# Kernel tuning notes

Measured on AMD Instinct MI355X. Metric: run time of the kernel, lower is better.

Reference implementation:

```python
import jax, jax.numpy as jnp
import numpy as np

T, C, H, S = 2048, 2048, 32, 64
H_KV = 8
L_MAA, L_DEC = 32, 64


def setup_inputs() -> dict:
    key = jax.random.key(0)
    ks = jax.random.split(key, 20)
    def n(k, shp, s=1.0):
        return jax.random.normal(k, shp, dtype=jnp.float32) * s
    sc = 0.02  # init scale for projection weights
    return dict(
        x=n(ks[0], (T, C)),
        state=jnp.zeros((1 + S, C), jnp.float32),
        new_starts=jnp.zeros((T,), bool),
        length=T,
        time_maa_x=n(ks[1], (C,), 0.1),
        time_maa_r=n(ks[2], (C,), 0.1),
        time_maa_k=n(ks[3], (C,), 0.1),
        time_maa_v=n(ks[4], (C,), 0.1),
        time_maa_w=n(ks[5], (C,), 0.1),
        time_maa_g=n(ks[6], (C,), 0.1),
        time_maa_w1=n(ks[7], (C, 5 * L_MAA), sc),
        time_maa_w2=n(ks[8], (5, L_MAA, C), sc),
        time_decay=n(ks[9], (C,), 0.5),
        time_decay_w1=n(ks[10], (C, L_DEC), sc),
        time_decay_w2=n(ks[11], (L_DEC, C), sc),
        Wq=n(ks[12], (C, H * S), sc),
        Wk=n(ks[13], (C, H_KV * S), sc),
        Wv=n(ks[14], (C, H_KV * S), sc),
        Wg=n(ks[15], (C, C), sc),
        Wo=n(ks[16], (C, C), sc),
    )


def reference(x, state, new_starts, length,
              time_maa_x, time_maa_r, time_maa_k, time_maa_v, time_maa_w, time_maa_g,
              time_maa_w1, time_maa_w2,
              time_decay, time_decay_w1, time_decay_w2,
              Wq, Wk, Wv, Wg, Wo):
    # token shift: previous token (state[0] for t=0), zeroed at sequence starts
    sx = jnp.concatenate([state[:1], x[:-1]], axis=0)
    sx = jnp.where(new_starts[:, None], 0.0, sx) - x  # [T, C]

    # data-dependent token-shift mix via LoRA (5 branches: r,k,v,w,g)
    xxx = x + sx * time_maa_x
    m = jnp.tanh(xxx @ time_maa_w1).reshape(T, 5, L_MAA).transpose(1, 0, 2)  # [5,T,L]
    m = jnp.einsum('ntl,nlc->ntc', m, time_maa_w2)  # [5,T,C]
    mr, mk, mv, mw, mg = m
    xr = x + sx * (time_maa_r + mr)
    xk = x + sx * (time_maa_k + mk)
    xv = x + sx * (time_maa_v + mv)
    xw = x + sx * (time_maa_w + mw)
    xg = x + sx * (time_maa_g + mg)

    new_state0 = x[length - 1]  # last valid token

    r = (xr @ Wq).reshape(T, H, S)
    k = (xk @ Wk).reshape(T, H_KV, S)
    v = (xv @ Wv).reshape(T, H_KV, S)

    # per-token decay via LoRA
    dec = time_decay.reshape(1, H, S) + (jnp.tanh(xw @ time_decay_w1) @ time_decay_w2).reshape(T, H, S)
    g = jax.nn.sigmoid(xg @ Wg)  # [T, C]

    reps = H // H_KV
    k = jnp.repeat(k, reps, axis=1)  # [T,H,S]
    v = jnp.repeat(v, reps, axis=1)

    log_w = jnp.maximum(-jnp.exp(dec), -5.0)  # [T,H,S]
    k = k * (1.0 - jnp.exp(log_w))

    s0 = state[1:].reshape(H, S, S)

    def step(s, inp):
        r_t, k_t, v_t, lw_t, ns_t = inp
        s = jnp.where(ns_t, 0.0, s)
        # decay along key dim, then rank-1 update k^T v
        s = s * jnp.exp(lw_t)[:, :, None] + k_t[:, :, None] * v_t[:, None, :]
        o = jnp.einsum('hk,hkv->hv', r_t, s)
        return s, o

    s_fin, out = jax.lax.scan(step, s0, (r, k, v, log_w, new_starts))

    new_state = state.at[0].set(new_state0).at[1:].set(s_fin.reshape(S, H * S))
    y = out.reshape(T, H * S) * g
    return y @ Wo, new_state
```

## Files before the change

### kernel.cpp

```cpp
#include <hip/hip_runtime.h>
#include <hip/hip_bf16.h>
#include <cmath>

#define T_DIM 2048
#define C_DIM 2048
#define NH    32
#define SS    64
#define NC    64
#define CL    32

typedef unsigned short ushort_t;
typedef __attribute__((ext_vector_type(8))) short bf16x8;
typedef __attribute__((ext_vector_type(4))) float f32x4;

__device__ __forceinline__ ushort_t f2bf(float v) {
    union { __hip_bfloat16 b; ushort_t u; } cv;
    cv.b = __float2bfloat16(v);
    return cv.u;
}

__device__ __forceinline__ void gload_lds16(const void* g, void* l) {
    __builtin_amdgcn_global_load_lds((const __attribute__((address_space(1))) void*)g,
                                     (__attribute__((address_space(3))) void*)l,
                                     16, 0, 0);
}

__device__ __forceinline__ float bcast(float x, int k) {
    return __int_as_float(__builtin_amdgcn_readlane(__float_as_int(x), k));
}

__global__ __launch_bounds__(256)
void mega_init(const float* __restrict__ W1, const float* __restrict__ Wd1,
               const float* __restrict__ Wd2, const float* __restrict__ Wq,
               const float* __restrict__ Wk, const float* __restrict__ Wv,
               const float* __restrict__ Wg, const float* __restrict__ W2,
               ushort_t* __restrict__ W1T, ushort_t* __restrict__ Wd1T,
               ushort_t* __restrict__ Wd2T, ushort_t* __restrict__ WqT,
               ushort_t* __restrict__ WkT, ushort_t* __restrict__ WvT,
               ushort_t* __restrict__ WgT, ushort_t* __restrict__ W2Tall,
               const float* __restrict__ x, const float* __restrict__ state,
               const unsigned char* __restrict__ ns, const float* __restrict__ tmx,
               float* __restrict__ sx, ushort_t* __restrict__ xxxb,
               const int* __restrict__ len, float* __restrict__ outstate) {
    __shared__ float t[32][33];
    int bx = blockIdx.x;
    int tid = threadIdx.x;

    if (bx < 4096) {
        int i4 = bx * 256 + tid;
        int idx = i4 * 4;
        int tt = idx >> 11;
        int c = idx & 2047;
        float4 xv = *(const float4*)(x + idx);
        float4 prev;
        if (ns[tt]) prev = make_float4(0.f, 0.f, 0.f, 0.f);
        else if (tt == 0) prev = *(const float4*)(state + c);
        else prev = *(const float4*)(x + idx - C_DIM);
        float4 tm = *(const float4*)(tmx + c);
        float4 s4;
        s4.x = prev.x - xv.x;  s4.y = prev.y - xv.y;
        s4.z = prev.z - xv.z;  s4.w = prev.w - xv.w;
        *(float4*)(sx + idx) = s4;
        ushort4 xb;
        xb.x = f2bf(xv.x + s4.x * tm.x);
        xb.y = f2bf(xv.y + s4.y * tm.y);
        xb.z = f2bf(xv.z + s4.z * tm.z);
        xb.w = f2bf(xv.w + s4.w * tm.w);
        *(ushort4*)(xxxb + idx) = xb;
        return;
    }
    bx -= 4096;
    if (bx < 8) {
        int c = bx * 256 + tid;
        if (c < C_DIM)
            outstate[c] = x[(size_t)(len[0] - 1) * C_DIM + c];
        return;
    }
    bx -= 8;
    const float* W; ushort_t* WT; int K, N, nx;
    if (bx < 512)        {            W = W1;  WT = W1T;  K = 2048; N = 160;  nx = 8;  }
    else if (bx < 768)   { bx -= 512; W = Wd1; WT = Wd1T; K = 2048; N = 64;   nx = 4;  }
    else if (bx < 896)   { bx -= 768; W = Wd2; WT = Wd2T; K = 64;   N = 2048; nx = 64; }
    else if (bx < 4992)  { bx -= 896; W = Wq;  WT = WqT;  K = 2048; N = 2048; nx = 64; }
    else if (bx < 6016)  { bx -= 4992; W = Wk; WT = WkT;  K = 2048; N = 512;  nx = 16; }
    else if (bx < 7040)  { bx -= 6016; W = Wv; WT = WvT;  K = 2048; N = 512;  nx = 16; }
    else if (bx < 11136) { bx -= 7040; W = Wg; WT = WgT;  K = 2048; N = 2048; nx = 64; }
    else {
        bx -= 11136;
        int br = bx >> 6; bx &= 63;
        W = W2 + (size_t)br * 32 * C_DIM; WT = W2Tall + (size_t)br * C_DIM * 32;
        K = 32; N = 2048; nx = 64;
    }
    int n0 = (bx % nx) * 32, k0 = (bx / nx) * 32;
    int tx = tid & 31, ty = tid >> 5;
    #pragma unroll
    for (int i = 0; i < 4; ++i) {
        int k = ty + i * 8;
        float v = 0.f;
        if (n0 + tx < N) v = W[(size_t)(k0 + k) * N + n0 + tx];
        t[k][tx] = v;
    }
    __syncthreads();
    #pragma unroll
    for (int i = 0; i < 4; ++i) {
        int n = ty + i * 8;
        WT[(size_t)(n0 + n) * K + k0 + tx] = f2bf(t[tx][n]);
    }
}

template<int EPI>
__global__ __launch_bounds__(256)
void gemm_mfma(const ushort_t* __restrict__ A, int lda,
               const ushort_t* __restrict__ BT,
               const float* __restrict__ bias,
               float* __restrict__ Cf, ushort_t* __restrict__ Cb,
               int ldc, int K) {
    __shared__ ushort_t As[2][128 * 32];
    __shared__ ushort_t Bs[2][128 * 32];
    int tid = threadIdx.x;
    int wave = tid >> 6, lane = tid & 63;
    int m0 = blockIdx.y * 128, n0 = blockIdx.x * 128;
    int wm = wave >> 1, wn = wave & 1;

    f32x4 acc[4][4] = {};

    int srow0 = wave * 16 + (lane >> 2);
    int schunk = lane & 3;

    int row0 = srow0, row1 = 64 + srow0;
    int gch0 = schunk ^ (row0 & 3), gch1 = schunk ^ (row1 & 3);
    const ushort_t* gA0 = A + (size_t)(m0 + row0) * lda + gch0 * 8;
    const ushort_t* gA1 = A + (size_t)(m0 + row1) * lda + gch1 * 8;
    const ushort_t* gB0 = BT + (size_t)(n0 + row0) * K + gch0 * 8;
    const ushort_t* gB1 = BT + (size_t)(n0 + row1) * K + gch1 * 8;
    int l0 = row0 * 32 + schunk * 8;
    int l1 = row1 * 32 + schunk * 8;

    int nt = K >> 5;

    gload_lds16(gA0, &As[0][l0]);
    gload_lds16(gB0, &Bs[0][l0]);
    gload_lds16(gA1, &As[0][l1]);
    gload_lds16(gB1, &Bs[0][l1]);
    __syncthreads();

    int fr = lane & 15;
    int fc = lane >> 4;
    int cur = 0;
    for (int t = 0; t < nt; ++t) {
        if (t + 1 < nt) {
            int k0 = (t + 1) << 5;
            gload_lds16(gA0 + k0, &As[cur ^ 1][l0]);
            gload_lds16(gB0 + k0, &Bs[cur ^ 1][l0]);
            gload_lds16(gA1 + k0, &As[cur ^ 1][l1]);
            gload_lds16(gB1 + k0, &Bs[cur ^ 1][l1]);
        }
        bf16x8 af[4], bfr[4];
        #pragma unroll
        for (int mi = 0; mi < 4; ++mi) {
            int r = wm * 64 + mi * 16 + fr;
            af[mi] = *(const bf16x8*)(&As[cur][r * 32 + ((fc ^ (r & 3)) * 8)]);
        }
        #pragma unroll
        for (int ni = 0; ni < 4; ++ni) {
            int c = wn * 64 + ni * 16 + fr;
            bfr[ni] = *(const bf16x8*)(&Bs[cur][c * 32 + ((fc ^ (c & 3)) * 8)]);
        }
        #pragma unroll
        for (int mi = 0; mi < 4; ++mi)
            #pragma unroll
            for (int ni = 0; ni < 4; ++ni)
                acc[mi][ni] = __builtin_amdgcn_mfma_f32_16x16x32_bf16(
                    af[mi], bfr[ni], acc[mi][ni], 0, 0, 0);
        __syncthreads();
        cur ^= 1;
    }

    int colin = lane & 15;
    int rquad = lane >> 4;
    #pragma unroll
    for (int mi = 0; mi < 4; ++mi) {
        #pragma unroll
        for (int reg = 0; reg < 4; ++reg) {
            int row = m0 + wm * 64 + mi * 16 + rquad * 4 + reg;
            #pragma unroll
            for (int ni = 0; ni < 4; ++ni) {
                int col = n0 + wn * 64 + ni * 16 + colin;
                float v = acc[mi][ni][reg];
                if (EPI == 2) v = 1.f / (1.f + __expf(-v));
                else if (EPI == 3) v += bias[col];
                else if (EPI == 4) v = tanhf(v);
                if (EPI == 4) Cb[(size_t)row * ldc + col] = f2bf(v);
                else          Cf[(size_t)row * ldc + col] = v;
            }
        }
    }
}

__global__ __launch_bounds__(256)
void gemm_fused5(const ushort_t* __restrict__ xw, const ushort_t* __restrict__ xk,
                 const ushort_t* __restrict__ xv, const ushort_t* __restrict__ xr,
                 const ushort_t* __restrict__ xg,
                 const ushort_t* __restrict__ Wd1T, const ushort_t* __restrict__ WkT,
                 const ushort_t* __restrict__ WvT, const ushort_t* __restrict__ WqT,
                 const ushort_t* __restrict__ WgT,
                 ushort_t* __restrict__ tw, float* __restrict__ k0g,
                 float* __restrict__ v0g, float* __restrict__ rg,
                 float* __restrict__ gg) {
    const int K = 2048, lda = 2048;
    int id = blockIdx.y * 41 + blockIdx.x;
    int swz = (id & 7) * 82 + (id >> 3);
    int bx = swz >> 4;
    int m0 = (swz & 15) * 128;

    const ushort_t* A; const ushort_t* BT;
    float* Cf = nullptr; ushort_t* Cb = nullptr;
    int ldc, n0, epi;
    if (bx == 0)       { A = xw; BT = Wd1T; Cb = tw;  ldc = 128;  n0 = 0;               epi = 4; }
    else if (bx < 5)   { A = xk; BT = WkT;  Cf = k0g; ldc = 512;  n0 = (bx - 1) * 128;  epi = 0; }
    else if (bx < 9)   { A = xv; BT = WvT;  Cf = v0g; ldc = 512;  n0 = (bx - 5) * 128;  epi = 0; }
    else if (bx < 25)  { A = xr; BT = WqT;  Cf = rg;  ldc = 2048; n0 = (bx - 9) * 128;  epi = 0; }
    else               { A = xg; BT = WgT;  Cf = gg;  ldc = 2048; n0 = (bx - 25) * 128; epi = 2; }

    __shared__ ushort_t As[2][128 * 32];
    __shared__ ushort_t Bs[2][128 * 32];
    int tid = threadIdx.x;
    int wave = tid >> 6, lane = tid & 63;
    int wm = wave >> 1, wn = wave & 1;

    f32x4 acc[4][4] = {};

    int srow0 = wave * 16 + (lane >> 2);
    int schunk = lane & 3;
    int row0 = srow0, row1 = 64 + srow0;
    int gch0 = schunk ^ (row0 & 3), gch1 = schunk ^ (row1 & 3);
    const ushort_t* gA0 = A + (size_t)(m0 + row0) * lda + gch0 * 8;
    const ushort_t* gA1 = A + (size_t)(m0 + row1) * lda + gch1 * 8;
    const ushort_t* gB0 = BT + (size_t)(n0 + row0) * K + gch0 * 8;
    const ushort_t* gB1 = BT + (size_t)(n0 + row1) * K + gch1 * 8;
    int l0 = row0 * 32 + schunk * 8;
    int l1 = row1 * 32 + schunk * 8;

    const int nt = K >> 5;
    gload_lds16(gA0, &As[0][l0]);
    gload_lds16(gB0, &Bs[0][l0]);
    gload_lds16(gA1, &As[0][l1]);
    gload_lds16(gB1, &Bs[0][l1]);
    __syncthreads();

    int fr = lane & 15;
    int fc = lane >> 4;
    int cur = 0;
    for (int t = 0; t < nt; ++t) {
        if (t + 1 < nt) {
            int kk = (t + 1) << 5;
            gload_lds16(gA0 + kk, &As[cur ^ 1][l0]);
            gload_lds16(gB0 + kk, &Bs[cur ^ 1][l0]);
            gload_lds16(gA1 + kk, &As[cur ^ 1][l1]);
            gload_lds16(gB1 + kk, &Bs[cur ^ 1][l1]);
        }
        bf16x8 af[4], bfr[4];
        #pragma unroll
        for (int mi = 0; mi < 4; ++mi) {
            int r = wm * 64 + mi * 16 + fr;
            af[mi] = *(const bf16x8*)(&As[cur][r * 32 + ((fc ^ (r & 3)) * 8)]);
        }
        #pragma unroll
        for (int ni = 0; ni < 4; ++ni) {
            int c = wn * 64 + ni * 16 + fr;
            bfr[ni] = *(const bf16x8*)(&Bs[cur][c * 32 + ((fc ^ (c & 3)) * 8)]);
        }
        #pragma unroll
        for (int mi = 0; mi < 4; ++mi)
            #pragma unroll
            for (int ni = 0; ni < 4; ++ni)
                acc[mi][ni] = __builtin_amdgcn_mfma_f32_16x16x32_bf16(
                    af[mi], bfr[ni], acc[mi][ni], 0, 0, 0);
        __syncthreads();
        cur ^= 1;
    }

    int colin = lane & 15;
    int rquad = lane >> 4;
    #pragma unroll
    for (int mi = 0; mi < 4; ++mi) {
        #pragma unroll
        for (int reg = 0; reg < 4; ++reg) {
            int row = m0 + wm * 64 + mi * 16 + rquad * 4 + reg;
            #pragma unroll
            for (int ni = 0; ni < 4; ++ni) {
                int col = n0 + wn * 64 + ni * 16 + colin;
                float v = acc[mi][ni][reg];
                if (epi == 2) v = 1.f / (1.f + __expf(-v));
                else if (epi == 4) v = tanhf(v);
                if (epi == 4) Cb[(size_t)row * ldc + col] = f2bf(v);
                else          Cf[(size_t)row * ldc + col] = v;
            }
        }
    }
}

__global__ __launch_bounds__(256)
void dec_cast(const ushort_t* __restrict__ tw, const ushort_t* __restrict__ Wd2T,
              const float* __restrict__ tdec, float* __restrict__ dec,
              const float* __restrict__ Wo, ushort_t* __restrict__ WoT) {
    int id = blockIdx.x;
    int tid = threadIdx.x;
    if (id >= 256) {
        __shared__ float t[32][33];
        int c = id - 256;
        int n0 = (c & 63) * 32, k0 = (c >> 6) * 32;
        int tx = tid & 31, ty = tid >> 5;
        #pragma unroll
        for (int i = 0; i < 4; ++i) {
            int k = ty + i * 8;
            t[k][tx] = Wo[(size_t)(k0 + k) * 2048 + n0 + tx];
        }
        __syncthreads();
        #pragma unroll
        for (int i = 0; i < 4; ++i) {
            int n = ty + i * 8;
            WoT[(size_t)(n0 + n) * 2048 + k0 + tx] = f2bf(t[tx][n]);
        }
        return;
    }
    const int K = 64, lda = 128, ldc = 2048;
    __shared__ ushort_t As[2][128 * 32];
    __shared__ ushort_t Bs[2][128 * 32];
    int wave = tid >> 6, lane = tid & 63;
    int m0 = (id >> 4) * 128, n0 = (id & 15) * 128;
    int wm = wave >> 1, wn = wave & 1;

    f32x4 acc[4][4] = {};
    int srow0 = wave * 16 + (lane >> 2);
    int schunk = lane & 3;
    int row0 = srow0, row1 = 64 + srow0;
    int gch0 = schunk ^ (row0 & 3), gch1 = schunk ^ (row1 & 3);
    const ushort_t* gA0 = tw + (size_t)(m0 + row0) * lda + gch0 * 8;
    const ushort_t* gA1 = tw + (size_t)(m0 + row1) * lda + gch1 * 8;
    const ushort_t* gB0 = Wd2T + (size_t)(n0 + row0) * K + gch0 * 8;
    const ushort_t* gB1 = Wd2T + (size_t)(n0 + row1) * K + gch1 * 8;
    int l0 = row0 * 32 + schunk * 8;
    int l1 = row1 * 32 + schunk * 8;

    const int nt = K >> 5;
    gload_lds16(gA0, &As[0][l0]);
    gload_lds16(gB0, &Bs[0][l0]);
    gload_lds16(gA1, &As[0][l1]);
    gload_lds16(gB1, &Bs[0][l1]);
    __syncthreads();

    int fr = lane & 15;
    int fc = lane >> 4;
    int cur = 0;
    for (int t = 0; t < nt; ++t) {
        if (t + 1 < nt) {
            int kk = (t + 1) << 5;
            gload_lds16(gA0 + kk, &As[cur ^ 1][l0]);
            gload_lds16(gB0 + kk, &Bs[cur ^ 1][l0]);
            gload_lds16(gA1 + kk, &As[cur ^ 1][l1]);
            gload_lds16(gB1 + kk, &Bs[cur ^ 1][l1]);
        }
        bf16x8 af[4], bfr[4];
        #pragma unroll
        for (int mi = 0; mi < 4; ++mi) {
            int r = wm * 64 + mi * 16 + fr;
            af[mi] = *(const bf16x8*)(&As[cur][r * 32 + ((fc ^ (r & 3)) * 8)]);
        }
        #pragma unroll
        for (int ni = 0; ni < 4; ++ni) {
            int c = wn * 64 + ni * 16 + fr;
            bfr[ni] = *(const bf16x8*)(&Bs[cur][c * 32 + ((fc ^ (c & 3)) * 8)]);
        }
        #pragma unroll
        for (int mi = 0; mi < 4; ++mi)
            #pragma unroll
            for (int ni = 0; ni < 4; ++ni)
                acc[mi][ni] = __builtin_amdgcn_mfma_f32_16x16x32_bf16(
                    af[mi], bfr[ni], acc[mi][ni], 0, 0, 0);
        __syncthreads();
        cur ^= 1;
    }

    int colin = lane & 15;
    int rquad = lane >> 4;
    #pragma unroll
    for (int mi = 0; mi < 4; ++mi) {
        #pragma unroll
        for (int reg = 0; reg < 4; ++reg) {
            int row = m0 + wm * 64 + mi * 16 + rquad * 4 + reg;
            #pragma unroll
            for (int ni = 0; ni < 4; ++ni) {
                int col = n0 + wn * 64 + ni * 16 + colin;
                dec[(size_t)row * ldc + col] = acc[mi][ni][reg] + tdec[col];
            }
        }
    }
}

__global__ __launch_bounds__(256)
void maa_gemm(const ushort_t* __restrict__ mtlb,
              const ushort_t* __restrict__ W2Tall,
              const float* __restrict__ x, const float* __restrict__ sx,
              const float* __restrict__ tmr, const float* __restrict__ tmk,
              const float* __restrict__ tmv, const float* __restrict__ tmw,
              const float* __restrict__ tmg,
              ushort_t* __restrict__ xr, ushort_t* __restrict__ xk,
              ushort_t* __restrict__ xv, ushort_t* __restrict__ xw,
              ushort_t* __restrict__ xg) {
    int br = blockIdx.z;
    const ushort_t* BT = W2Tall + (size_t)br * C_DIM * 32;
    const float* tm; ushort_t* dst;
    if      (br == 0) { tm = tmr; dst = xr; }
    else if (br == 1) { tm = tmk; dst = xk; }
    else if (br == 2) { tm = tmv; dst = xv; }
    else if (br == 3) { tm = tmw; dst = xw; }
    else              { tm = tmg; dst = xg; }

    __shared__ ushort_t As[128 * 32];
    __shared__ ushort_t Bs[128 * 32];
    int tid = threadIdx.x;
    int wave = tid >> 6, lane = tid & 63;
    int m0 = blockIdx.y * 128, n0 = blockIdx.x * 128;
    int wm = wave >> 1, wn = wave & 1;
    int srow0 = wave * 16 + (lane >> 2);
    int schunk = lane & 3;

    #pragma unroll
    for (int j = 0; j < 2; ++j) {
        int row = j * 64 + srow0;
        int gch = schunk ^ (row & 3);
        gload_lds16(mtlb + (size_t)(m0 + row) * 256 + br * 32 + gch * 8,
                    As + row * 32 + schunk * 8);
        gload_lds16(BT + (size_t)(n0 + row) * 32 + gch * 8,
                    Bs + row * 32 + schunk * 8);
    }
    __syncthreads();

    int fr = lane & 15;
    int fc = lane >> 4;
    f32x4 acc[4][4] = {};
    bf16x8 af[4], bfr[4];
    #pragma unroll
    for (int mi = 0; mi < 4; ++mi) {
        int r = wm * 64 + mi * 16 + fr;
        af[mi] = *(const bf16x8*)(As + r * 32 + ((fc ^ (r & 3)) * 8));
    }
    #pragma unroll
    for (int ni = 0; ni < 4; ++ni) {
        int c = wn * 64 + ni * 16 + fr;
        bfr[ni] = *(const bf16x8*)(Bs + c * 32 + ((fc ^ (c & 3)) * 8));
    }
    #pragma unroll
    for (int mi = 0; mi < 4; ++mi)
        #pragma unroll
        for (int ni = 0; ni < 4; ++ni)
            acc[mi][ni] = __builtin_amdgcn_mfma_f32_16x16x32_bf16(
                af[mi], bfr[ni], acc[mi][ni], 0, 0, 0);

    int colin = lane & 15;
    int rquad = lane >> 4;
    #pragma unroll
    for (int mi = 0; mi < 4; ++mi) {
        #pragma unroll
        for (int reg = 0; reg < 4; ++reg) {
            int row = m0 + wm * 64 + mi * 16 + rquad * 4 + reg;
            #pragma unroll
            for (int ni = 0; ni < 4; ++ni) {
                int col = n0 + wn * 64 + ni * 16 + colin;
                size_t idx = (size_t)row * C_DIM + col;
                float m = acc[mi][ni][reg];
                dst[idx] = f2bf(x[idx] + sx[idx] * (tm[col] + m));
            }
        }
    }
}

__global__ __launch_bounds__(64)
void scan_pass1(const float* __restrict__ k0, const float* __restrict__ v0,
                const float* __restrict__ dec, const unsigned char* __restrict__ ns,
                float* __restrict__ U, float* __restrict__ P) {
    int h = blockIdx.x, c = blockIdx.y, v = threadIdx.x;
    int hk = h >> 2;
    float u[64];
    #pragma unroll
    for (int k = 0; k < 64; ++k) u[k] = 0.f;
    float pk = 1.f;
    int t0 = c * CL;
    float dv_n = dec[(size_t)t0 * 2048 + h * 64 + v];
    float kv_n = k0[(size_t)t0 * 512 + hk * 64 + v];
    float vv_n = v0[(size_t)t0 * 512 + hk * 64 + v];
    unsigned char ns_n = ns[t0];
    for (int i = 0; i < CL; ++i) {
        float dv = dv_n, kv = kv_n, vv = vv_n;
        unsigned char nsv = ns_n;
        if (i + 1 < CL) {
            int t = t0 + i + 1;
            dv_n = dec[(size_t)t * 2048 + h * 64 + v];
            kv_n = k0[(size_t)t * 512 + hk * 64 + v];
            vv_n = v0[(size_t)t * 512 + hk * 64 + v];
            ns_n = ns[t];
        }
        float lw = fmaxf(-__expf(dv), -5.f);
        float ew = __expf(lw);
        float ewp = nsv ? 0.f : ew;
        float kk = kv * (1.f - ew);
        pk *= ewp;
        #pragma unroll
        for (int k = 0; k < 64; ++k) {
            float ewk = bcast(ewp, k);
            float kkk = bcast(kk, k);
            u[k] = fmaf(u[k], ewk, kkk * vv);
        }
    }
    size_t base = ((size_t)h * NC + c) * 4096;
    #pragma unroll
    for (int k = 0; k < 64; ++k) U[base + k * 64 + v] = u[k];
    P[((size_t)h * NC + c) * 64 + v] = pk;
}

__global__ __launch_bounds__(256)
void scan_pass2(float* __restrict__ U, const float* __restrict__ P,
                const float* __restrict__ state, float* __restrict__ outstate) {
    int e = blockIdx.x * 256 + threadIdx.x;
    int h = e >> 12;
    int k = (e >> 6) & 63;
    float s = state[C_DIM + e];
    int rem = e & 4095;
    #pragma unroll 4
    for (int c = 0; c < NC; ++c) {
        size_t ub = ((size_t)h * NC + c) * 4096 + rem;
        float p = P[((size_t)h * NC + c) * 64 + k];
        float u = U[ub];
        U[ub] = s;
        s = fmaf(s, p, u);
    }
    outstate[C_DIM + e] = s;
}

__global__ __launch_bounds__(64)
void scan_pass3(const float* __restrict__ r, const float* __restrict__ k0,
                const float* __restrict__ v0, const float* __restrict__ dec,
                const unsigned char* __restrict__ ns,
                const float* __restrict__ Sstarts, const float* __restrict__ g,
                ushort_t* __restrict__ y0b) {
    int h = blockIdx.x, c = blockIdx.y, v = threadIdx.x;
    int hk = h >> 2;
    float s[64];
    size_t base = ((size_t)h * NC + c) * 4096;
    #pragma unroll
    for (int k = 0; k < 64; ++k) s[k] = Sstarts[base + k * 64 + v];
    int t0 = c * CL;
    float dv_n = dec[(size_t)t0 * 2048 + h * 64 + v];
    float kv_n = k0[(size_t)t0 * 512 + hk * 64 + v];
    float vv_n = v0[(size_t)t0 * 512 + hk * 64 + v];
    float rr_n = r[(size_t)t0 * 2048 + h * 64 + v];
    float gg_n = g[(size_t)t0 * 2048 + h * 64 + v];
    unsigned char ns_n = ns[t0];
    for (int i = 0; i < CL; ++i) {
        float dv = dv_n, kv = kv_n, vv = vv_n, rr = rr_n, gg = gg_n;
        unsigned char nsv = ns_n;
        if (i + 1 < CL) {
            int t = t0 + i + 1;
            dv_n = dec[(size_t)t * 2048 + h * 64 + v];
            kv_n = k0[(size_t)t * 512 + hk * 64 + v];
            vv_n = v0[(size_t)t * 512 + hk * 64 + v];
            rr_n = r[(size_t)t * 2048 + h * 64 + v];
            gg_n = g[(size_t)t * 2048 + h * 64 + v];
            ns_n = ns[t];
        }
        float lw = fmaxf(-__expf(dv), -5.f);
        float ew = __expf(lw);
        float ewl = nsv ? 0.f : ew;
        float kkl = kv * (1.f - ew);
        float o0 = 0.f, o1 = 0.f, o2 = 0.f, o3 = 0.f;
        #pragma unroll
        for (int k = 0; k < 64; k += 4) {
            float s0 = fmaf(s[k],     bcast(ewl, k),     bcast(kkl, k)     * vv); s[k]     = s0; o0 = fmaf(bcast(rr, k),     s0, o0);
            float s1 = fmaf(s[k + 1], bcast(ewl, k + 1), bcast(kkl, k + 1) * vv); s[k + 1] = s1; o1 = fmaf(bcast(rr, k + 1), s1, o1);
            float s2 = fmaf(s[k + 2], bcast(ewl, k + 2), bcast(kkl, k + 2) * vv); s[k + 2] = s2; o2 = fmaf(bcast(rr, k + 2), s2, o2);
            float s3 = fmaf(s[k + 3], bcast(ewl, k + 3), bcast(kkl, k + 3) * vv); s[k + 3] = s3; o3 = fmaf(bcast(rr, k + 3), s3, o3);
        }
        float o = (o0 + o1) + (o2 + o3);
        size_t idx = (size_t)(t0 + i) * 2048 + h * 64 + v;
        y0b[idx] = f2bf(o * gg);
    }
}

extern "C" void kernel_launch(void* const* d_in, const int* in_sizes, int n_in,
                              void* d_out, int out_size, void* d_ws, size_t ws_size,
                              hipStream_t stream) {
    const float* x     = (const float*)d_in[0];
    const float* state = (const float*)d_in[1];
    const unsigned char* ns = (const unsigned char*)d_in[2];
    const int*   len   = (const int*)d_in[3];
    const float* tmx   = (const float*)d_in[4];
    const float* tmr   = (const float*)d_in[5];
    const float* tmk   = (const float*)d_in[6];
    const float* tmv   = (const float*)d_in[7];
    const float* tmw   = (const float*)d_in[8];
    const float* tmg   = (const float*)d_in[9];
    const float* W1    = (const float*)d_in[10];
    const float* W2    = (const float*)d_in[11];
    const float* tdec  = (const float*)d_in[12];
    const float* Wd1   = (const float*)d_in[13];
    const float* Wd2   = (const float*)d_in[14];
    const float* Wq    = (const float*)d_in[15];
    const float* Wk    = (const float*)d_in[16];
    const float* Wv    = (const float*)d_in[17];
    const float* Wg    = (const float*)d_in[18];
    const float* Wo    = (const float*)d_in[19];

    float* out = (float*)d_out;
    float* outstate = out + (size_t)T_DIM * C_DIM;

    char* wsb = (char*)d_ws;
    const size_t MB = 1024 * 1024;
    float*    sx   = (float*)(wsb + 0);
    float*    g    = (float*)(wsb + 0);
    ushort_t* xxxb = (ushort_t*)(wsb + 16 * MB);
    ushort_t* mtlb = (ushort_t*)(wsb + 24 * MB);
    ushort_t* tw   = (ushort_t*)(wsb + 25 * MB);
    float*    P    = (float*)(wsb + 25 * MB + 512 * 1024);
    ushort_t* xr   = (ushort_t*)(wsb + 26 * MB);
    ushort_t* xk   = (ushort_t*)(wsb + 34 * MB);
    float*    dec  = (float*)(wsb + 26 * MB);
    ushort_t* xv   = (ushort_t*)(wsb + 42 * MB);
    ushort_t* WoT  = (ushort_t*)(wsb + 42 * MB);
    ushort_t* xw   = (ushort_t*)(wsb + 50 * MB);
    ushort_t* xg   = (ushort_t*)(wsb + 58 * MB);
    float*    r    = (float*)(wsb + 66 * MB);
    float*    k0   = (float*)(wsb + 82 * MB);
    float*    v0   = (float*)(wsb + 86 * MB);
    ushort_t* WqT  = (ushort_t*)(wsb + 90 * MB);
    ushort_t* WkT  = (ushort_t*)(wsb + 98 * MB);
    ushort_t* WvT  = (ushort_t*)(wsb + 100 * MB);
    ushort_t* W1T  = (ushort_t*)(wsb + 102 * MB);
    ushort_t* Wd1T = (ushort_t*)(wsb + 103 * MB);
    ushort_t* Wd2T = (ushort_t*)(wsb + 103 * MB + 512 * 1024);
    ushort_t* W2Tall = (ushort_t*)(wsb + 104 * MB);
    ushort_t* WgT  = (ushort_t*)(wsb + 106 * MB);
    float*    U    = (float*)(wsb + 90 * MB);
    ushort_t* y0b  = xxxb;

    dim3 blk(256);

    mega_init<<<dim3(15560), blk, 0, stream>>>(
        W1, Wd1, Wd2, Wq, Wk, Wv, Wg, W2,
        W1T, Wd1T, Wd2T, WqT, WkT, WvT, WgT, W2Tall,
        x, state, ns, tmx, sx, xxxb, len, outstate);

    gemm_mfma<4><<<dim3(2, 16), blk, 0, stream>>>(xxxb, 2048, W1T, nullptr, nullptr, mtlb, 256, 2048);
    maa_gemm<<<dim3(16, 16, 5), blk, 0, stream>>>(mtlb, W2Tall, x, sx,
                                                  tmr, tmk, tmv, tmw, tmg,
                                                  xr, xk, xv, xw, xg);
    gemm_fused5<<<dim3(41, 16), blk, 0, stream>>>(xw, xk, xv, xr, xg,
                                                  Wd1T, WkT, WvT, WqT, WgT,
                                                  tw, k0, v0, r, g);
    dec_cast<<<dim3(4352), blk, 0, stream>>>(tw, Wd2T, tdec, dec, Wo, WoT);
    scan_pass1<<<dim3(NH, NC), dim3(64), 0, stream>>>(k0, v0, dec, ns, U, P);
    scan_pass2<<<dim3(512), blk, 0, stream>>>(U, P, state, outstate);
    scan_pass3<<<dim3(NH, NC), dim3(64), 0, stream>>>(r, k0, v0, dec, ns, U, g, y0b);
    gemm_mfma<0><<<dim3(16, 16), blk, 0, stream>>>(y0b, 2048, WoT, nullptr, out, nullptr, 2048, 2048);
}
```

Baseline: 474.1 us.

## Split-K the W1 LoRA GEMM, retile Wo GEMM blocks by XCD, change LDS swizzle

The small W1 GEMM (2048x256, K=2048) previously ran on only 32 blocks. It is now split along K into 8 slices writing fp32 partials, followed by a reduce kernel that sums the slices and applies tanh with a bf16 cast. This is meant to fill the GPU with more blocks. The Wo GEMM gets a block-index remap that groups tiles per XCD for L2 locality, and every GEMM switches to a new XOR swizzle for LDS reads to cut bank conflicts. The cost is extra partial traffic plus one more kernel launch.

```diff
diff --git a/kernel.cpp b/kernel.cpp
--- a/kernel.cpp
+++ b/kernel.cpp
@@ -8,6 +8,8 @@
 #define SS    64
 #define NC    64
 #define CL    32
+
+#define SWZ(r) (((r) + ((r) >> 2)) & 3)
 
 typedef unsigned short ushort_t;
 typedef __attribute__((ext_vector_type(8))) short bf16x8;
@@ -108,27 +110,120 @@
     }
 }
 
-template<int EPI>
 __global__ __launch_bounds__(256)
-void gemm_mfma(const ushort_t* __restrict__ A, int lda,
+void w1_splitk(const ushort_t* __restrict__ A,
                const ushort_t* __restrict__ BT,
-               const float* __restrict__ bias,
-               float* __restrict__ Cf, ushort_t* __restrict__ Cb,
-               int ldc, int K) {
+               float* __restrict__ Wp) {
+    const int lda = 2048, K = 2048;
     __shared__ ushort_t As[2][128 * 32];
     __shared__ ushort_t Bs[2][128 * 32];
     int tid = threadIdx.x;
     int wave = tid >> 6, lane = tid & 63;
     int m0 = blockIdx.y * 128, n0 = blockIdx.x * 128;
+    int kbase = blockIdx.z * 256;
+    float* Cf = Wp + (size_t)blockIdx.z * 2048 * 256;
     int wm = wave >> 1, wn = wave & 1;
 
     f32x4 acc[4][4] = {};
-
     int srow0 = wave * 16 + (lane >> 2);
     int schunk = lane & 3;
-
     int row0 = srow0, row1 = 64 + srow0;
-    int gch0 = schunk ^ (row0 & 3), gch1 = schunk ^ (row1 & 3);
+    int gch0 = schunk ^ SWZ(row0), gch1 = schunk ^ SWZ(row1);
+    const ushort_t* gA0 = A + (size_t)(m0 + row0) * lda + kbase + gch0 * 8;
+    const ushort_t* gA1 = A + (size_t)(m0 + row1) * lda + kbase + gch1 * 8;
+    const ushort_t* gB0 = BT + (size_t)(n0 + row0) * K + kbase + gch0 * 8;
+    const ushort_t* gB1 = BT + (size_t)(n0 + row1) * K + kbase + gch1 * 8;
+    int l0 = row0 * 32 + schunk * 8;
+    int l1 = row1 * 32 + schunk * 8;
+
+    const int nt = 8;
+    gload_lds16(gA0, &As[0][l0]);
+    gload_lds16(gB0, &Bs[0][l0]);
+    gload_lds16(gA1, &As[0][l1]);
+    gload_lds16(gB1, &Bs[0][l1]);
+    __syncthreads();
+
+    int fr = lane & 15;
+    int fc = lane >> 4;
+    int cur = 0;
+    for (int t = 0; t < nt; ++t) {
+        if (t + 1 < nt) {
+            int kk = (t + 1) << 5;
+            gload_lds16(gA0 + kk, &As[cur ^ 1][l0]);
+            gload_lds16(gB0 + kk, &Bs[cur ^ 1][l0]);
+            gload_lds16(gA1 + kk, &As[cur ^ 1][l1]);
+            gload_lds16(gB1 + kk, &Bs[cur ^ 1][l1]);
+        }
+        bf16x8 af[4], bfr[4];
+        #pragma unroll
+        for (int mi = 0; mi < 4; ++mi) {
+            int r = wm * 64 + mi * 16 + fr;
+            af[mi] = *(const bf16x8*)(&As[cur][r * 32 + ((fc ^ SWZ(r)) * 8)]);
+        }
+        #pragma unroll
+        for (int ni = 0; ni < 4; ++ni) {
+            int c = wn * 64 + ni * 16 + fr;
+            bfr[ni] = *(const bf16x8*)(&Bs[cur][c * 32 + ((fc ^ SWZ(c)) * 8)]);
+        }
+        #pragma unroll
+        for (int mi = 0; mi < 4; ++mi)
+            #pragma unroll
+            for (int ni = 0; ni < 4; ++ni)
+                acc[mi][ni] = __builtin_amdgcn_mfma_f32_16x16x32_bf16(
+                    af[mi], bfr[ni], acc[mi][ni], 0, 0, 0);
+        __syncthreads();
+        cur ^= 1;
+    }
+
+    int colin = lane & 15;
+    int rquad = lane >> 4;
+    #pragma unroll
+    for (int mi = 0; mi < 4; ++mi)
+        #pragma unroll
+        for (int reg = 0; reg < 4; ++reg) {
+            int row = m0 + wm * 64 + mi * 16 + rquad * 4 + reg;
+            #pragma unroll
+            for (int ni = 0; ni < 4; ++ni) {
+                int col = n0 + wn * 64 + ni * 16 + colin;
+                Cf[(size_t)row * 256 + col] = acc[mi][ni][reg];
+            }
+        }
+}
+
+__global__ __launch_bounds__(256)
+void w1_reduce(const float* __restrict__ Wp, ushort_t* __restrict__ mtlb) {
+    int idx = (blockIdx.x * 256 + threadIdx.x) * 4;
+    float4 s = *(const float4*)(Wp + idx);
+    #pragma unroll
+    for (int z = 1; z < 8; ++z) {
+        float4 p = *(const float4*)(Wp + (size_t)z * 2048 * 256 + idx);
+        s.x += p.x; s.y += p.y; s.z += p.z; s.w += p.w;
+    }
+    ushort4 o;
+    o.x = f2bf(tanhf(s.x)); o.y = f2bf(tanhf(s.y));
+    o.z = f2bf(tanhf(s.z)); o.w = f2bf(tanhf(s.w));
+    *(ushort4*)(mtlb + idx) = o;
+}
+
+__global__ __launch_bounds__(256)
+void gemm_wo(const ushort_t* __restrict__ A, const ushort_t* __restrict__ BT,
+             float* __restrict__ Cf) {
+    const int lda = 2048, K = 2048, ldc = 2048;
+    __shared__ ushort_t As[2][128 * 32];
+    __shared__ ushort_t Bs[2][128 * 32];
+    int tid = threadIdx.x;
+    int wave = tid >> 6, lane = tid & 63;
+    int id = blockIdx.y * 16 + blockIdx.x;
+    int xcd = id & 7, j = id >> 3;
+    int m0 = ((xcd >> 1) * 4 + (j & 3)) * 128;
+    int n0 = ((xcd & 1) * 8 + (j >> 2)) * 128;
+    int wm = wave >> 1, wn = wave & 1;
+
+    f32x4 acc[4][4] = {};
+    int srow0 = wave * 16 + (lane >> 2);
+    int schunk = lane & 3;
+    int row0 = srow0, row1 = 64 + srow0;
+    int gch0 = schunk ^ SWZ(row0), gch1 = schunk ^ SWZ(row1);
     const ushort_t* gA0 = A + (size_t)(m0 + row0) * lda + gch0 * 8;
     const ushort_t* gA1 = A + (size_t)(m0 + row1) * lda + gch1 * 8;
     const ushort_t* gB0 = BT + (size_t)(n0 + row0) * K + gch0 * 8;
@@ -136,8 +231,7 @@
     int l0 = row0 * 32 + schunk * 8;
     int l1 = row1 * 32 + schunk * 8;
 
-    int nt = K >> 5;
-
+    const int nt = K >> 5;
     gload_lds16(gA0, &As[0][l0]);
     gload_lds16(gB0, &Bs[0][l0]);
     gload_lds16(gA1, &As[0][l1]);
@@ -149,22 +243,22 @@
     int cur = 0;
     for (int t = 0; t < nt; ++t) {
         if (t + 1 < nt) {
-            int k0 = (t + 1) << 5;
-            gload_lds16(gA0 + k0, &As[cur ^ 1][l0]);
-            gload_lds16(gB0 + k0, &Bs[cur ^ 1][l0]);
-            gload_lds16(gA1 + k0, &As[cur ^ 1][l1]);
-            gload_lds16(gB1 + k0, &Bs[cur ^ 1][l1]);
+            int kk = (t + 1) << 5;
+            gload_lds16(gA0 + kk, &As[cur ^ 1][l0]);
+            gload_lds16(gB0 + kk, &Bs[cur ^ 1][l0]);
+            gload_lds16(gA1 + kk, &As[cur ^ 1][l1]);
+            gload_lds16(gB1 + kk, &Bs[cur ^ 1][l1]);
         }
         bf16x8 af[4], bfr[4];
         #pragma unroll
         for (int mi = 0; mi < 4; ++mi) {
             int r = wm * 64 + mi * 16 + fr;
-            af[mi] = *(const bf16x8*)(&As[cur][r * 32 + ((fc ^ (r & 3)) * 8)]);
+            af[mi] = *(const bf16x8*)(&As[cur][r * 32 + ((fc ^ SWZ(r)) * 8)]);
         }
         #pragma unroll
         for (int ni = 0; ni < 4; ++ni) {
             int c = wn * 64 + ni * 16 + fr;
-            bfr[ni] = *(const bf16x8*)(&Bs[cur][c * 32 + ((fc ^ (c & 3)) * 8)]);
+            bfr[ni] = *(const bf16x8*)(&Bs[cur][c * 32 + ((fc ^ SWZ(c)) * 8)]);
         }
         #pragma unroll
         for (int mi = 0; mi < 4; ++mi)
@@ -179,22 +273,16 @@
     int colin = lane & 15;
     int rquad = lane >> 4;
     #pragma unroll
-    for (int mi = 0; mi < 4; ++mi) {
+    for (int mi = 0; mi < 4; ++mi)
         #pragma unroll
         for (int reg = 0; reg < 4; ++reg) {
             int row = m0 + wm * 64 + mi * 16 + rquad * 4 + reg;
             #pragma unroll
             for (int ni = 0; ni < 4; ++ni) {
                 int col = n0 + wn * 64 + ni * 16 + colin;
-                float v = acc[mi][ni][reg];
-                if (EPI == 2) v = 1.f / (1.f + __expf(-v));
-                else if (EPI == 3) v += bias[col];
-                else if (EPI == 4) v = tanhf(v);
-                if (EPI == 4) Cb[(size_t)row * ldc + col] = f2bf(v);
-                else          Cf[(size_t)row * ldc + col] = v;
+                Cf[(size_t)row * ldc + col] = acc[mi][ni][reg];
             }
         }
-    }
 }
 
 __global__ __launch_bounds__(256)
@@ -229,11 +317,10 @@
     int wm = wave >> 1, wn = wave & 1;
 
     f32x4 acc[4][4] = {};
-
     int srow0 = wave * 16 + (lane >> 2);
     int schunk = lane & 3;
     int row0 = srow0, row1 = 64 + srow0;
-    int gch0 = schunk ^ (row0 & 3), gch1 = schunk ^ (row1 & 3);
+    int gch0 = schunk ^ SWZ(row0), gch1 = schunk ^ SWZ(row1);
     const ushort_t* gA0 = A + (size_t)(m0 + row0) * lda + gch0 * 8;
     const ushort_t* gA1 = A + (size_t)(m0 + row1) * lda + gch1 * 8;
     const ushort_t* gB0 = BT + (size_t)(n0 + row0) * K + gch0 * 8;
@@ -263,12 +350,12 @@
         #pragma unroll
         for (int mi = 0; mi < 4; ++mi) {
             int r = wm * 64 + mi * 16 + fr;
-            af[mi] = *(const bf16x8*)(&As[cur][r * 32 + ((fc ^ (r & 3)) * 8)]);
+            af[mi] = *(const bf16x8*)(&As[cur][r * 32 + ((fc ^ SWZ(r)) * 8)]);
         }
         #pragma unroll
         for (int ni = 0; ni < 4; ++ni) {
             int c = wn * 64 + ni * 16 + fr;
-            bfr[ni] = *(const bf16x8*)(&Bs[cur][c * 32 + ((fc ^ (c & 3)) * 8)]);
+            bfr[ni] = *(const bf16x8*)(&Bs[cur][c * 32 + ((fc ^ SWZ(c)) * 8)]);
         }
         #pragma unroll
         for (int mi = 0; mi < 4; ++mi)
@@ -335,7 +422,7 @@
     int srow0 = wave * 16 + (lane >> 2);
     int schunk = lane & 3;
     int row0 = srow0, row1 = 64 + srow0;
-    int gch0 = schunk ^ (row0 & 3), gch1 = schunk ^ (row1 & 3);
+    int gch0 = schunk ^ SWZ(row0), gch1 = schunk ^ SWZ(row1);
     const ushort_t* gA0 = tw + (size_t)(m0 + row0) * lda + gch0 * 8;
     const ushort_t* gA1 = tw + (size_t)(m0 + row1) * lda + gch1 * 8;
     const ushort_t* gB0 = Wd2T + (size_t)(n0 + row0) * K + gch0 * 8;
@@ -365,12 +452,12 @@
         #pragma unroll
         for (int mi = 0; mi < 4; ++mi) {
             int r = wm * 64 + mi * 16 + fr;
-            af[mi] = *(const bf16x8*)(&As[cur][r * 32 + ((fc ^ (r & 3)) * 8)]);
+            af[mi] = *(const bf16x8*)(&As[cur][r * 32 + ((fc ^ SWZ(r)) * 8)]);
         }
         #pragma unroll
         for (int ni = 0; ni < 4; ++ni) {
             int c = wn * 64 + ni * 16 + fr;
-            bfr[ni] = *(const bf16x8*)(&Bs[cur][c * 32 + ((fc ^ (c & 3)) * 8)]);
+            bfr[ni] = *(const bf16x8*)(&Bs[cur][c * 32 + ((fc ^ SWZ(c)) * 8)]);
         }
         #pragma unroll
         for (int mi = 0; mi < 4; ++mi)
@@ -385,7 +472,7 @@
     int colin = lane & 15;
     int rquad = lane >> 4;
     #pragma unroll
-    for (int mi = 0; mi < 4; ++mi) {
+    for (int mi = 0; mi < 4; ++mi)
         #pragma unroll
         for (int reg = 0; reg < 4; ++reg) {
             int row = m0 + wm * 64 + mi * 16 + rquad * 4 + reg;
@@ -395,7 +482,6 @@
                 dec[(size_t)row * ldc + col] = acc[mi][ni][reg] + tdec[col];
             }
         }
-    }
 }
 
 __global__ __launch_bounds__(256)
@@ -429,7 +515,7 @@
     #pragma unroll
     for (int j = 0; j < 2; ++j) {
         int row = j * 64 + srow0;
-        int gch = schunk ^ (row & 3);
+        int gch = schunk ^ SWZ(row);
         gload_lds16(mtlb + (size_t)(m0 + row) * 256 + br * 32 + gch * 8,
                     As + row * 32 + schunk * 8);
         gload_lds16(BT + (size_t)(n0 + row) * 32 + gch * 8,
@@ -444,12 +530,12 @@
     #pragma unroll
     for (int mi = 0; mi < 4; ++mi) {
         int r = wm * 64 + mi * 16 + fr;
-        af[mi] = *(const bf16x8*)(As + r * 32 + ((fc ^ (r & 3)) * 8));
+        af[mi] = *(const bf16x8*)(As + r * 32 + ((fc ^ SWZ(r)) * 8));
     }
     #pragma unroll
     for (int ni = 0; ni < 4; ++ni) {
         int c = wn * 64 + ni * 16 + fr;
-        bfr[ni] = *(const bf16x8*)(Bs + c * 32 + ((fc ^ (c & 3)) * 8));
+        bfr[ni] = *(const bf16x8*)(Bs + c * 32 + ((fc ^ SWZ(c)) * 8));
     }
     #pragma unroll
     for (int mi = 0; mi < 4; ++mi)
@@ -630,6 +716,7 @@
     ushort_t* xw   = (ushort_t*)(wsb + 50 * MB);
     ushort_t* xg   = (ushort_t*)(wsb + 58 * MB);
     float*    r    = (float*)(wsb + 66 * MB);
+    float*    Wp   = (float*)(wsb + 66 * MB);
     float*    k0   = (float*)(wsb + 82 * MB);
     float*    v0   = (float*)(wsb + 86 * MB);
     ushort_t* WqT  = (ushort_t*)(wsb + 90 * MB);
@@ -650,7 +737,8 @@
         W1T, Wd1T, Wd2T, WqT, WkT, WvT, WgT, W2Tall,
         x, state, ns, tmx, sx, xxxb, len, outstate);
 
-    gemm_mfma<4><<<dim3(2, 16), blk, 0, stream>>>(xxxb, 2048, W1T, nullptr, nullptr, mtlb, 256, 2048);
+    w1_splitk<<<dim3(2, 16, 8), blk, 0, stream>>>(xxxb, W1T, Wp);
+    w1_reduce<<<dim3(512), blk, 0, stream>>>(Wp, mtlb);
     maa_gemm<<<dim3(16, 16, 5), blk, 0, stream>>>(mtlb, W2Tall, x, sx,
                                                   tmr, tmk, tmv, tmw, tmg,
                                                   xr, xk, xv, xw, xg);
@@ -661,5 +749,5 @@
     scan_pass1<<<dim3(NH, NC), dim3(64), 0, stream>>>(k0, v0, dec, ns, U, P);
     scan_pass2<<<dim3(512), blk, 0, stream>>>(U, P, state, outstate);
     scan_pass3<<<dim3(NH, NC), dim3(64), 0, stream>>>(r, k0, v0, dec, ns, U, g, y0b);
-    gemm_mfma<0><<<dim3(16, 16), blk, 0, stream>>>(y0b, 2048, WoT, nullptr, out, nullptr, 2048, 2048);
-}
+    gemm_wo<<<dim3(16, 16), blk, 0, stream>>>(y0b, WoT, out);
+}
```

Measured after the change: 448.5 us. -5.4%, faster.
